# Kernel optimization log

Hardware: AMD Instinct MI355X
Metric: run time of the kernel (lower is better)

## Reference

```python
import jax, jax.numpy as jnp
import numpy as np

B, N = 4, 2466  # batch, vertex count (Pixel2Mesh stage-3 mesh)
IMG = 224.0


def _vertex_align(feat_maps, pos):
    """Bilinear-style gather of image features at projected vertex locations.
    feat_maps: list of [B,C,S,S]; pos: [B,N,3]. Returns [B,N,sum(C)]."""
    z = pos[..., 2]
    h = jnp.clip(248.0 * (pos[..., 1] / z) + 111.5, 0.0, 223.0)
    w = jnp.clip(248.0 * (pos[..., 0] / (-z)) + 111.5, 0.0, 223.0)
    outs = []
    for f in feat_maps:
        S = f.shape[-1]
        x = h / (IMG / S)
        y = w / (IMG / S)
        x1 = jnp.floor(x).astype(jnp.int32)
        x2 = jnp.minimum(jnp.ceil(x).astype(jnp.int32), S - 1)
        y1 = jnp.floor(y).astype(jnp.int32)
        y2 = jnp.minimum(jnp.ceil(y).astype(jnp.int32), S - 1)
        xi = x.astype(jnp.int32)  # trunc == floor since x >= 0
        yi = y.astype(jnp.int32)

        def gat(fm, xs, ys):  # fm [C,S,S], xs/ys [N] -> [N,C]
            return fm[:, xs, ys].T

        g = jax.vmap(gat)
        w11 = ((x2 - xi) * (y2 - yi)).astype(f.dtype)[..., None]
        w12 = ((x2 - xi) * (yi - y1)).astype(f.dtype)[..., None]
        w21 = ((xi - x1) * (y2 - yi)).astype(f.dtype)[..., None]
        w22 = ((xi - x1) * (yi - y1)).astype(f.dtype)[..., None]
        outs.append(w11 * g(f, x1, y1) + w21 * g(f, x2, y1)
                    + w12 * g(f, x1, y2) + w22 * g(f, x2, y2))
    return jnp.concatenate(outs, axis=-1)


def _graph_conv(x, adj, w0, w1):
    # relu(X @ w0 + A @ (X @ w1))
    return jax.nn.relu(x @ w0 + jnp.einsum('bmn,bnc->bmc', adj, x @ w1))


def _res_graph_conv(x, adj, pw, pb, w00, w01, w10, w11):
    skip = x @ pw + pb
    out = _graph_conv(x, adj, w00, w01)
    out = _graph_conv(out, adj, w10, w11)
    return skip + out


def _forward(conv2_3, conv3_4, conv4_6, conv5_3, vertex_positions, vertex_features,
             vertex_adjacency, lin_w, lin_b,
             r0_pw, r0_pb, r0_w00, r0_w01, r0_w10, r0_w11,
             r1_pw, r1_pb, r1_w00, r1_w01, r1_w10, r1_w11,
             r2_pw, r2_pb, r2_w00, r2_w01, r2_w10, r2_w11,
             gf_w0, gf_w1):
    aligned = _vertex_align([conv2_3, conv3_4, conv4_6, conv5_3], vertex_positions)  # [B,N,3840]
    proj = aligned @ lin_w + lin_b  # [B,N,128]
    x = jnp.concatenate([proj, vertex_features, vertex_positions], axis=-1)  # [B,N,259]
    x = _res_graph_conv(x, vertex_adjacency, r0_pw, r0_pb, r0_w00, r0_w01, r0_w10, r0_w11)
    x = _res_graph_conv(x, vertex_adjacency, r1_pw, r1_pb, r1_w00, r1_w01, r1_w10, r1_w11)
    x = _res_graph_conv(x, vertex_adjacency, r2_pw, r2_pb, r2_w00, r2_w01, r2_w10, r2_w11)
    offset = jnp.tanh(_graph_conv(x, vertex_adjacency, gf_w0, gf_w1))  # [B,N,3]
    return vertex_positions + offset


def setup_inputs() -> dict:
    key = jax.random.key(0)
    ks = jax.random.split(key, 40)
    inp = {
        "conv2_3": jax.random.normal(ks[0], (B, 256, 56, 56), jnp.float32),
        "conv3_4": jax.random.normal(ks[1], (B, 512, 28, 28), jnp.float32),
        "conv4_6": jax.random.normal(ks[2], (B, 1024, 14, 14), jnp.float32),
        "conv5_3": jax.random.normal(ks[3], (B, 2048, 7, 7), jnp.float32),
        "vertex_positions": jax.random.normal(ks[4], (B, N, 3), jnp.float32),
        "vertex_features": jax.random.normal(ks[5], (B, N, 128), jnp.float32),
        # sparse 0/1 adjacency stored dense (the torch module uses dense bmm)
        "vertex_adjacency": (jax.random.uniform(ks[6], (B, N, N)) < 0.003).astype(jnp.float32),
    }

    def u(k, shape, fan):
        b = 1.0 / np.sqrt(fan)
        return jax.random.uniform(k, shape, jnp.float32, -b, b)

    specs = [("lin_w", (3840, 128), 3840), ("lin_b", (128,), 3840)]
    for j, ci in enumerate([259, 128, 128]):
        p = f"r{j}_"
        specs += [(p + "pw", (ci, 128), ci), (p + "pb", (128,), ci),
                  (p + "w00", (ci, 128), ci), (p + "w01", (ci, 128), ci),
                  (p + "w10", (128, 128), 128), (p + "w11", (128, 128), 128)]
    specs += [("gf_w0", (128, 3), 128), ("gf_w1", (128, 3), 128)]
    for i, (name, shape, fan) in enumerate(specs):
        inp[name] = u(ks[7 + i], shape, fan)
    return inp


def reference(conv2_3, conv3_4, conv4_6, conv5_3, vertex_positions, vertex_features,
              vertex_adjacency, lin_w, lin_b,
              r0_pw, r0_pb, r0_w00, r0_w01, r0_w10, r0_w11,
              r1_pw, r1_pb, r1_w00, r1_w01, r1_w10, r1_w11,
              r2_pw, r2_pb, r2_w00, r2_w01, r2_w10, r2_w11,
              gf_w0, gf_w1):
    return _forward(conv2_3, conv3_4, conv4_6, conv5_3, vertex_positions, vertex_features,
                    vertex_adjacency, lin_w, lin_b,
                    r0_pw, r0_pb, r0_w00, r0_w01, r0_w10, r0_w11,
                    r1_pw, r1_pb, r1_w00, r1_w01, r1_w10, r1_w11,
                    r2_pw, r2_pb, r2_w00, r2_w01, r2_w10, r2_w11,
                    gf_w0, gf_w1)
```

## Files before the change

kernel.cpp:

```cpp
#include <hip/hip_runtime.h>
#include <cmath>

#define B_   4
#define N_   2466
#define R_   (B_*N_)
#define ELLW 96

typedef _Float16 f16x8 __attribute__((ext_vector_type(8)));
typedef __attribute__((ext_vector_type(4))) float f32x4;

__device__ __forceinline__ unsigned short f16_bits(float x) {
  union { _Float16 h; unsigned short u; } c;
  c.h = (_Float16)x;
  return c.u;
}

struct WMats { const float* p[15]; };


__global__ __launch_bounds__(256) void k_pre(
    const float* __restrict__ c2, const float* __restrict__ c3,
    const float* __restrict__ c4, const float* __restrict__ c5,
    unsigned short* __restrict__ t0, unsigned short* __restrict__ t1,
    unsigned short* __restrict__ t2, unsigned short* __restrict__ t3,
    const float* __restrict__ adj, int* __restrict__ cols, int* __restrict__ cnts,
    const float* __restrict__ lin_w,
    unsigned short* __restrict__ whf,
    WMats wm,
    unsigned short* __restrict__ wrf) {
  __shared__ float t[64][66];
  int bid = blockIdx.x;
  int tid = threadIdx.x;
  if (bid < 1584) {
    const float* in; unsigned short* out; int C, P, npb, ncb, rem;
    if (bid < 784)       { in = c2; out = t0; C = 256;  P = 3136; npb = 49; ncb = 4;  rem = bid; }
    else if (bid < 1200) { in = c3; out = t1; C = 512;  P = 784;  npb = 13; ncb = 8;  rem = bid - 784; }
    else if (bid < 1456) { in = c4; out = t2; C = 1024; P = 196;  npb = 4;  ncb = 16; rem = bid - 1200; }
    else                 { in = c5; out = t3; C = 2048; P = 49;   npb = 1;  ncb = 32; rem = bid - 1456; }
    int pb = rem % npb; int tq = rem / npb; int cb = tq % ncb; int b = tq / ncb;
    int c0 = cb * 64, p0 = pb * 64;
    #pragma unroll
    for (int i = 0; i < 8; i++) {
      int e = tid + i * 256;
      int c = e >> 5, f2 = e & 31;
      int p = p0 + f2 * 2;
      float2 v = make_float2(0.f, 0.f);
      const float* src = in + ((size_t)b * C + (c0 + c)) * P + p;
      if (p + 1 < P)      v = *(const float2*)src;
      else if (p < P)     v.x = *src;
      *(float2*)&t[c][f2 * 2] = v;
    }
    __syncthreads();
    int jj = tid & 15, c4i = jj * 4;
    #pragma unroll
    for (int pass = 0; pass < 4; pass++) {
      int pp = pass * 16 + (tid >> 4);
      int px = p0 + pp;
      if (px < P) {
        ushort4 o;
        o.x = f16_bits(t[c4i + 0][pp]);
        o.y = f16_bits(t[c4i + 1][pp]);
        o.z = f16_bits(t[c4i + 2][pp]);
        o.w = f16_bits(t[c4i + 3][pp]);
        *(ushort4*)&out[((size_t)b * P + px) * C + c0 + c4i] = o;
      }
    }
  } else if (bid < 4050) {
    int wave = tid >> 6, lane = tid & 63;
    int row = (bid - 1584) * 4 + wave;
    const float* Ar = adj + (size_t)row * N_;
    int* cp = cols + (size_t)row * ELLW;
    unsigned long long below = (lane == 63) ? 0xFFFFFFFFFFFFFFFFull >> 1
                                            : ((1ull << lane) - 1ull);
    float4 v[10];
    #pragma unroll
    for (int i0 = 0; i0 < 10; i0++) {
      int j0 = i0 * 256 + lane * 4;
      if (j0 + 3 < N_) {
        v[i0] = *(const float4*)&Ar[j0];
      } else {
        v[i0] = make_float4(0.f, 0.f, 0.f, 0.f);
        if (j0     < N_) v[i0].x = Ar[j0];
        if (j0 + 1 < N_) v[i0].y = Ar[j0+1];
        if (j0 + 2 < N_) v[i0].z = Ar[j0+2];
      }
    }
    int base = 0;
    #pragma unroll
    for (int i0 = 0; i0 < 10; i0++) {
      int j0 = i0 * 256 + lane * 4;
      bool nz0 = (j0     < N_) && (v[i0].x != 0.f);
      bool nz1 = (j0 + 1 < N_) && (v[i0].y != 0.f);
      bool nz2 = (j0 + 2 < N_) && (v[i0].z != 0.f);
      bool nz3 = (j0 + 3 < N_) && (v[i0].w != 0.f);
      unsigned long long m0 = __ballot(nz0);
      unsigned long long m1 = __ballot(nz1);
      unsigned long long m2 = __ballot(nz2);
      unsigned long long m3 = __ballot(nz3);
      int pre = __popcll(m0 & below) + __popcll(m1 & below)
              + __popcll(m2 & below) + __popcll(m3 & below);
      int p0 = base + pre;
      int p1 = p0 + (nz0 ? 1 : 0);
      int p2 = p1 + (nz1 ? 1 : 0);
      int p3 = p2 + (nz2 ? 1 : 0);
      if (nz0 && p0 < ELLW) cp[p0] = j0;
      if (nz1 && p1 < ELLW) cp[p1] = j0 + 1;
      if (nz2 && p2 < ELLW) cp[p2] = j0 + 2;
      if (nz3 && p3 < ELLW) cp[p3] = j0 + 3;
      base += __popcll(m0) + __popcll(m1) + __popcll(m2) + __popcll(m3);
    }
    if (lane == 0) cnts[row] = (base > ELLW) ? ELLW : base;
  } else if (bid < 4530) {
    int b = bid - 4050;
    int e0 = (b * 256 + tid) * 4;
    #pragma unroll
    for (int u = 0; u < 4; u++) {
      int e = e0 + u;
      int j = e & 7;
      int lane = (e >> 3) & 63;
      int nt = (e >> 9) & 7;
      int slab = e >> 12;
      int k = slab * 32 + ((lane >> 4) << 3) + j;
      int n = nt * 16 + (lane & 15);
      whf[e] = f16_bits(lin_w[(size_t)k * 128 + n]);
    }
  } else {
    int b = bid - 4530;
    int e0 = (b * 256 + tid) * 4;
    #pragma unroll
    for (int u = 0; u < 4; u++) {
      int e = e0 + u;
      int rb, mat, rem, K;
      if (e < 143360) {
        rb = 0;
        if (e < 110592) { mat = e / 36864; rem = e - mat * 36864; K = 259; }
        else { int tt = e - 110592; mat = 3 + tt / 16384; rem = tt & 16383; K = 128; }
      } else {
        int tt = e - 143360;
        rb = 1 + tt / 81920;
        int r2 = tt % 81920;
        mat = r2 / 16384; rem = r2 & 16383; K = 128;
      }
      int j = rem & 7, lane = (rem >> 3) & 63, nt = (rem >> 9) & 7, slab = rem >> 12;
      int k = slab * 32 + ((lane >> 4) << 3) + j;
      int n = nt * 16 + (lane & 15);
      float x = (k < K) ? wm.p[rb * 5 + mat][(size_t)k * 128 + n] : 0.f;
      wrf[e] = f16_bits(x);
    }
  }
}

__global__ __launch_bounds__(512) void k_align_mfma(
    const unsigned short* __restrict__ tr0, const unsigned short* __restrict__ tr1,
    const unsigned short* __restrict__ tr2, const unsigned short* __restrict__ tr3,
    const float* __restrict__ pos,
    const unsigned short* __restrict__ whf,
    float* __restrict__ part, int kchunk) {
  int tid  = threadIdx.x;
  int wave = tid >> 6, lane = tid & 63;
  int q    = lane >> 4, l15 = lane & 15;
  int m0   = blockIdx.x * 128;
  int s    = blockIdx.y;
  int mrow = m0 + wave * 16 + l15;

  int zero[4]; int base[4];
  {
    int rowc = (mrow < R_) ? mrow : 0;
    int b = rowc / N_;
    float px = pos[rowc*3+0], py = pos[rowc*3+1], pz = pos[rowc*3+2];
    float hh = fminf(fmaxf(248.f*(py/pz)    + 111.5f, 0.f), 223.f);
    float wc = fminf(fmaxf(248.f*(px/(-pz)) + 111.5f, 0.f), 223.f);
    const int Sarr[4] = {56, 28, 14, 7};
    const int Carr[4] = {256, 512, 1024, 2048};
    #pragma unroll
    for (int sc = 0; sc < 4; sc++) {
      int S = Sarr[sc], C = Carr[sc];
      float dv = 224.f / (float)S;
      float x = hh / dv, y = wc / dv;
      int x1 = (int)floorf(x), y1 = (int)floorf(y);
      int x2 = min((int)ceilf(x), S - 1), y2 = min((int)ceilf(y), S - 1);
      int w = (x2 - x1) * (y2 - y1);
      zero[sc] = (mrow >= R_) || (w == 0);
      base[sc] = (b * S * S + x1 * S + y1) * C;
    }
  }

  f32x4 acc[8];
  #pragma unroll
  for (int nt = 0; nt < 8; nt++) acc[nt] = (f32x4){0.f, 0.f, 0.f, 0.f};

  const f16x8* BH = (const f16x8*)whf;

  int kbeg = s * kchunk, kend = kbeg + kchunk;
  #pragma unroll 1
  for (int k0 = kbeg; k0 < kend; k0 += 32) {
    const unsigned short* tr; int off, sI;
    if (k0 < 256)       { tr = tr0; off = 0;    sI = 0; }
    else if (k0 < 768)  { tr = tr1; off = 256;  sI = 1; }
    else if (k0 < 1792) { tr = tr2; off = 768;  sI = 2; }
    else                { tr = tr3; off = 1792; sI = 3; }

    f16x8 af = *(const f16x8*)(tr + base[sI] + (k0 - off) + q * 8);
    if (zero[sI]) af = (f16x8)(_Float16)0;

    int slab = k0 >> 5;
    f16x8 Bh[8];
    #pragma unroll
    for (int nt = 0; nt < 8; nt++)
      Bh[nt] = BH[(size_t)(slab * 8 + nt) * 64 + lane];
    #pragma unroll
    for (int nt = 0; nt < 8; nt++)
      acc[nt] = __builtin_amdgcn_mfma_f32_16x16x32_f16(af, Bh[nt], acc[nt], 0, 0, 0);
  }

  #pragma unroll
  for (int nt = 0; nt < 8; nt++)
    #pragma unroll
    for (int r = 0; r < 4; r++) {
      int row = m0 + wave * 16 + q * 4 + r;
      if (row < R_)
        part[((size_t)s * R_ + row) * 128 + nt * 16 + l15] = acc[nt][r];
    }
}

__global__ __launch_bounds__(256) void k_reduce(
    const float* __restrict__ part, const float* __restrict__ lin_b,
    const float* __restrict__ vf, const float* __restrict__ pos,
    float* __restrict__ xcat, int nsplit) {
  int grp = threadIdx.x >> 5, ln = threadIdx.x & 31;
  int row = blockIdx.x * 8 + grp;
  float4 acc = ((const float4*)lin_b)[ln];
  for (int s = 0; s < nsplit; s++) {
    float4 pv = ((const float4*)part)[((size_t)s * R_ + row) * 32 + ln];
    acc.x += pv.x; acc.y += pv.y; acc.z += pv.z; acc.w += pv.w;
  }
  float4* xr = (float4*)(xcat + (size_t)row * 288);
  xr[ln] = acc;
  xr[32 + ln] = ((const float4*)vf)[(size_t)row * 32 + ln];
  if (ln < 8) {
    float4 z = make_float4(0.f, 0.f, 0.f, 0.f);
    if (ln == 0) {
      z.x = pos[(size_t)row * 3 + 0];
      z.y = pos[(size_t)row * 3 + 1];
      z.z = pos[(size_t)row * 3 + 2];
    }
    xr[64 + ln] = z;
  }
}

template<int SLABS>
__global__ __launch_bounds__(256) void k_gemm_mfma(
    const float* __restrict__ X, int ldx,
    const unsigned short* __restrict__ wf,
    int matStride, const float* __restrict__ pb,
    float* __restrict__ o0, float* __restrict__ o1, float* __restrict__ o2) {
  int tid = threadIdx.x;
  int wave = tid >> 6, lane = tid & 63;
  int q = lane >> 4, l15 = lane & 15;
  int which = blockIdx.y;
  int m0 = blockIdx.x * 64;
  int mrow = m0 + wave * 16 + l15;
  int rowc = (mrow < R_) ? mrow : (R_ - 1);
  const float* xrow = X + (size_t)rowc * ldx + q * 8;

  const f16x8* BH = (const f16x8*)(wf + (size_t)which * matStride);

  f32x4 acc[8];
  #pragma unroll
  for (int nt = 0; nt < 8; nt++) acc[nt] = (f32x4){0.f, 0.f, 0.f, 0.f};

  #pragma unroll 1
  for (int slab = 0; slab < SLABS; slab++) {
    const float* src = xrow + slab * 32;
    float4 a0 = *(const float4*)src;
    float4 a1 = *(const float4*)(src + 4);
    f16x8 af;
    af[0] = (_Float16)a0.x; af[1] = (_Float16)a0.y;
    af[2] = (_Float16)a0.z; af[3] = (_Float16)a0.w;
    af[4] = (_Float16)a1.x; af[5] = (_Float16)a1.y;
    af[6] = (_Float16)a1.z; af[7] = (_Float16)a1.w;
    f16x8 Bh[8];
    #pragma unroll
    for (int nt = 0; nt < 8; nt++)
      Bh[nt] = BH[(size_t)(slab * 8 + nt) * 64 + lane];
    #pragma unroll
    for (int nt = 0; nt < 8; nt++)
      acc[nt] = __builtin_amdgcn_mfma_f32_16x16x32_f16(af, Bh[nt], acc[nt], 0, 0, 0);
  }

  float* out = (which == 0) ? o0 : (which == 1) ? o1 : o2;
  #pragma unroll
  for (int nt = 0; nt < 8; nt++) {
    int col = nt * 16 + l15;
    float bias = (pb != nullptr && which == 2) ? pb[col] : 0.f;
    #pragma unroll
    for (int r = 0; r < 4; r++) {
      int row = m0 + wave * 16 + q * 4 + r;
      if (row < R_) out[(size_t)row * 128 + col] = acc[nt][r] + bias;
    }
  }
}

__global__ __launch_bounds__(256) void k_spmm(
    const float* __restrict__ sb, const float* __restrict__ tb,
    const int* __restrict__ cols, const int* __restrict__ cnts,
    const float* __restrict__ skipb, float* __restrict__ outb,
    const float* __restrict__ gw0, const float* __restrict__ gw1,
    float* __restrict__ gsb, float* __restrict__ gtb, int fuse_gf) {
  int tid = threadIdx.x;
  int grp = tid >> 5, ln = tid & 31;
  int row = blockIdx.x * 8 + grp;
  int b = row / N_;
  size_t tbase = (size_t)b * N_;
  const float4* sb4 = (const float4*)sb;
  const float4* tb4 = (const float4*)tb;
  const int* cp = cols + (size_t)row * ELLW;
  int4 ci0 = *(const int4*)cp;
  int4 ci1 = *(const int4*)(cp + 4);
  int cnt = cnts[row];
  float4 acc = sb4[(size_t)row*32 + ln];
  int idx[8] = {ci0.x, ci0.y, ci0.z, ci0.w, ci1.x, ci1.y, ci1.z, ci1.w};
  float4 g[8];
  #pragma unroll
  for (int i = 0; i < 8; i++) {
    int c = idx[i];
    c = (c >= 0 && c < N_) ? c : 0;
    g[i] = tb4[(tbase + c)*32 + ln];
  }
  #pragma unroll
  for (int i = 0; i < 8; i++) {
    if (i < cnt) {
      acc.x += g[i].x; acc.y += g[i].y; acc.z += g[i].z; acc.w += g[i].w;
    }
  }
  for (int i = 8; i < cnt; i++) {
    float4 v = tb4[(tbase + cp[i])*32 + ln];
    acc.x += v.x; acc.y += v.y; acc.z += v.z; acc.w += v.w;
  }
  acc.x = fmaxf(acc.x, 0.f); acc.y = fmaxf(acc.y, 0.f);
  acc.z = fmaxf(acc.z, 0.f); acc.w = fmaxf(acc.w, 0.f);
  if (skipb) {
    float4 sv = ((const float4*)skipb)[(size_t)row*32 + ln];
    acc.x += sv.x; acc.y += sv.y; acc.z += sv.z; acc.w += sv.w;
  }
  if (!fuse_gf) {
    ((float4*)outb)[(size_t)row*32 + ln] = acc;
    return;
  }
  float av[4] = {acc.x, acc.y, acc.z, acc.w};
  int j0 = ln * 4;
  float p0 = 0.f, p1 = 0.f, p2 = 0.f, q0 = 0.f, q1 = 0.f, q2 = 0.f;
  #pragma unroll
  for (int u = 0; u < 4; u++) {
    int j = j0 + u;
    p0 += av[u] * gw0[j*3+0]; p1 += av[u] * gw0[j*3+1]; p2 += av[u] * gw0[j*3+2];
    q0 += av[u] * gw1[j*3+0]; q1 += av[u] * gw1[j*3+1]; q2 += av[u] * gw1[j*3+2];
  }
  #pragma unroll
  for (int off = 16; off >= 1; off >>= 1) {
    p0 += __shfl_xor(p0, off); p1 += __shfl_xor(p1, off); p2 += __shfl_xor(p2, off);
    q0 += __shfl_xor(q0, off); q1 += __shfl_xor(q1, off); q2 += __shfl_xor(q2, off);
  }
  if (ln == 0) {
    gsb[(size_t)row*128 + 0] = p0; gsb[(size_t)row*128 + 1] = p1; gsb[(size_t)row*128 + 2] = p2;
    gtb[(size_t)row*128 + 0] = q0; gtb[(size_t)row*128 + 1] = q1; gtb[(size_t)row*128 + 2] = q2;
  }
}

__global__ __launch_bounds__(256) void k_gf_final(
    const float* __restrict__ sb, const float* __restrict__ tb,
    const int* __restrict__ cols, const int* __restrict__ cnts,
    const float* __restrict__ pos, float* __restrict__ out) {
  int wave = threadIdx.x >> 6, lane = threadIdx.x & 63;
  int row = blockIdx.x * 4 + wave;
  if (lane >= 3) return;
  int b = row / N_;
  float acc = sb[(size_t)row*128 + lane];
  int cnt = cnts[row];
  const int* cp = cols + (size_t)row * ELLW;
  size_t tbase = (size_t)b * N_;
  for (int i = 0; i < cnt; i++)
    acc += tb[(tbase + cp[i])*128 + lane];
  float v = tanhf(fmaxf(acc, 0.f));
  out[(size_t)row*3 + lane] = pos[(size_t)row*3 + lane] + v;
}

extern "C" void kernel_launch(void* const* d_in, const int* in_sizes, int n_in,
                              void* d_out, int out_size, void* d_ws, size_t ws_size,
                              hipStream_t stream) {
  const float* conv2_3 = (const float*)d_in[0];
  const float* conv3_4 = (const float*)d_in[1];
  const float* conv4_6 = (const float*)d_in[2];
  const float* conv5_3 = (const float*)d_in[3];
  const float* pos     = (const float*)d_in[4];
  const float* vf      = (const float*)d_in[5];
  const float* adj     = (const float*)d_in[6];
  const float* lin_w   = (const float*)d_in[7];
  const float* lin_b   = (const float*)d_in[8];
  const float* r_pb[3]  = {(const float*)d_in[10], (const float*)d_in[16], (const float*)d_in[22]};
  const float* gf_w0 = (const float*)d_in[27];
  const float* gf_w1 = (const float*)d_in[28];
  float* out = (float*)d_out;

  const size_t TRH_TOT = 6021120;
  const size_t ROWF    = (size_t)R_ * 128;
  const size_t XCAT_F  = (size_t)R_ * 288;
  const size_t LINW_E  = 491520;
  const size_t RESW_E  = 307200;

  unsigned short* trh0 = (unsigned short*)d_ws;
  unsigned short* trh1 = trh0 + (size_t)4*256*3136;
  unsigned short* trh2 = trh1 + (size_t)4*512*784;
  unsigned short* trh3 = trh2 + (size_t)4*1024*196;
  int*   ell_cnt  = (int*)(trh3 + (size_t)4*2048*49);
  int*   ell_cols = ell_cnt + R_;
  unsigned short* whf = (unsigned short*)(ell_cols + (size_t)R_*ELLW);
  unsigned short* wrf = whf + LINW_E;
  float* part = (float*)(wrf + RESW_E + 512);

  size_t fixed_f = TRH_TOT/2 + (size_t)R_*(ELLW+1) + (LINW_E + RESW_E + 512)/2;
  size_t need8 = (fixed_f + (size_t)8*ROWF + XCAT_F + 5*ROWF) * sizeof(float);
  int nsplit = (ws_size >= need8) ? 8 : 4;
  int kchunk = 3840 / nsplit;

  float* xcat = part + (size_t)nsplit * ROWF;
  float* sb   = xcat + XCAT_F;
  float* tb   = sb   + ROWF;
  float* skip = tb   + ROWF;
  float* hb   = skip + ROWF;
  float* xc   = hb   + ROWF;

  WMats wm;
  for (int rb = 0; rb < 3; rb++) {
    wm.p[rb*5 + 0] = (const float*)d_in[11 + 6*rb];
    wm.p[rb*5 + 1] = (const float*)d_in[12 + 6*rb];
    wm.p[rb*5 + 2] = (const float*)d_in[9  + 6*rb];
    wm.p[rb*5 + 3] = (const float*)d_in[13 + 6*rb];
    wm.p[rb*5 + 4] = (const float*)d_in[14 + 6*rb];
  }
  const int RB_BASE[3] = {0, 143360, 225280};

  k_pre<<<4830, 256, 0, stream>>>(conv2_3, conv3_4, conv4_6, conv5_3,
                                  trh0, trh1, trh2, trh3,
                                  adj, ell_cols, ell_cnt,
                                  lin_w, whf, wm, wrf);

  k_align_mfma<<<dim3(78, nsplit), 512, 0, stream>>>(trh0, trh1, trh2, trh3, pos,
                                                     whf, part, kchunk);

  k_reduce<<<1233, 256, 0, stream>>>(part, lin_b, vf, pos, xcat, nsplit);

  for (int rb = 0; rb < 3; rb++) {
    if (rb == 0) {
      k_gemm_mfma<9><<<dim3(155, 3), 256, 0, stream>>>(
          xcat, 288, wrf + RB_BASE[0], 36864, r_pb[0], sb, tb, skip);
    } else {
      k_gemm_mfma<4><<<dim3(155, 3), 256, 0, stream>>>(
          xc, 128, wrf + RB_BASE[rb], 16384, r_pb[rb], sb, tb, skip);
    }
    k_spmm<<<1233, 256, 0, stream>>>(sb, tb, ell_cols, ell_cnt, nullptr, hb,
                                     nullptr, nullptr, nullptr, nullptr, 0);
    int g2off = RB_BASE[rb] + ((rb == 0) ? 110592 : 3 * 16384);
    k_gemm_mfma<4><<<dim3(155, 2), 256, 0, stream>>>(
        hb, 128, wrf + g2off, 16384, nullptr, sb, tb, nullptr);
    if (rb < 2) {
      k_spmm<<<1233, 256, 0, stream>>>(sb, tb, ell_cols, ell_cnt, skip, xc,
                                       nullptr, nullptr, nullptr, nullptr, 0);
    } else {
      k_spmm<<<1233, 256, 0, stream>>>(sb, tb, ell_cols, ell_cnt, skip, nullptr,
                                       gf_w0, gf_w1, hb, xc, 1);
    }
  }

  k_gf_final<<<2466, 256, 0, stream>>>(hb, xc, ell_cols, ell_cnt, pos, out);
}
```

Before: 428.1 us.

## Process two row tiles per wave in align GEMM and prefetch more ELL neighbors

The vertex-align MFMA kernel now runs 4 waves per block, each covering two 16-row tiles, so every B-fragment load from the weight matrix feeds two MFMAs. This halves redundant weight traffic per row and raises the number of independent MFMAs in flight per wave, at the cost of more accumulator registers. The SpMM and final graph-conv kernels also issue 12 neighbor gathers up front instead of 8 (or a serial loop), to expose more memory-level parallelism for typical vertex degrees.

```diff
diff --git a/kernel.cpp b/kernel.cpp
--- a/kernel.cpp
+++ b/kernel.cpp
@@ -150,7 +150,7 @@
   }
 }
 
-__global__ __launch_bounds__(512) void k_align_mfma(
+__global__ __launch_bounds__(256) void k_align_mfma(
     const unsigned short* __restrict__ tr0, const unsigned short* __restrict__ tr1,
     const unsigned short* __restrict__ tr2, const unsigned short* __restrict__ tr3,
     const float* __restrict__ pos,
@@ -161,10 +161,11 @@
   int q    = lane >> 4, l15 = lane & 15;
   int m0   = blockIdx.x * 128;
   int s    = blockIdx.y;
-  int mrow = m0 + wave * 16 + l15;
-
-  int zero[4]; int base[4];
-  {
+
+  int zero[2][4]; int base[2][4];
+  #pragma unroll
+  for (int u = 0; u < 2; u++) {
+    int mrow = m0 + (wave * 2 + u) * 16 + l15;
     int rowc = (mrow < R_) ? mrow : 0;
     int b = rowc / N_;
     float px = pos[rowc*3+0], py = pos[rowc*3+1], pz = pos[rowc*3+2];
@@ -180,14 +181,16 @@
       int x1 = (int)floorf(x), y1 = (int)floorf(y);
       int x2 = min((int)ceilf(x), S - 1), y2 = min((int)ceilf(y), S - 1);
       int w = (x2 - x1) * (y2 - y1);
-      zero[sc] = (mrow >= R_) || (w == 0);
-      base[sc] = (b * S * S + x1 * S + y1) * C;
-    }
-  }
-
-  f32x4 acc[8];
-  #pragma unroll
-  for (int nt = 0; nt < 8; nt++) acc[nt] = (f32x4){0.f, 0.f, 0.f, 0.f};
+      zero[u][sc] = (mrow >= R_) || (w == 0);
+      base[u][sc] = (b * S * S + x1 * S + y1) * C;
+    }
+  }
+
+  f32x4 acc[2][8];
+  #pragma unroll
+  for (int u = 0; u < 2; u++)
+    #pragma unroll
+    for (int nt = 0; nt < 8; nt++) acc[u][nt] = (f32x4){0.f, 0.f, 0.f, 0.f};
 
   const f16x8* BH = (const f16x8*)whf;
 
@@ -200,8 +203,12 @@
     else if (k0 < 1792) { tr = tr2; off = 768;  sI = 2; }
     else                { tr = tr3; off = 1792; sI = 3; }
 
-    f16x8 af = *(const f16x8*)(tr + base[sI] + (k0 - off) + q * 8);
-    if (zero[sI]) af = (f16x8)(_Float16)0;
+    f16x8 af[2];
+    #pragma unroll
+    for (int u = 0; u < 2; u++) {
+      af[u] = *(const f16x8*)(tr + base[u][sI] + (k0 - off) + q * 8);
+      if (zero[u][sI]) af[u] = (f16x8)(_Float16)0;
+    }
 
     int slab = k0 >> 5;
     f16x8 Bh[8];
@@ -209,18 +216,22 @@
     for (int nt = 0; nt < 8; nt++)
       Bh[nt] = BH[(size_t)(slab * 8 + nt) * 64 + lane];
     #pragma unroll
+    for (int nt = 0; nt < 8; nt++) {
+      acc[0][nt] = __builtin_amdgcn_mfma_f32_16x16x32_f16(af[0], Bh[nt], acc[0][nt], 0, 0, 0);
+      acc[1][nt] = __builtin_amdgcn_mfma_f32_16x16x32_f16(af[1], Bh[nt], acc[1][nt], 0, 0, 0);
+    }
+  }
+
+  #pragma unroll
+  for (int u = 0; u < 2; u++)
+    #pragma unroll
     for (int nt = 0; nt < 8; nt++)
-      acc[nt] = __builtin_amdgcn_mfma_f32_16x16x32_f16(af, Bh[nt], acc[nt], 0, 0, 0);
-  }
-
-  #pragma unroll
-  for (int nt = 0; nt < 8; nt++)
-    #pragma unroll
-    for (int r = 0; r < 4; r++) {
-      int row = m0 + wave * 16 + q * 4 + r;
-      if (row < R_)
-        part[((size_t)s * R_ + row) * 128 + nt * 16 + l15] = acc[nt][r];
-    }
+      #pragma unroll
+      for (int r = 0; r < 4; r++) {
+        int row = m0 + (wave * 2 + u) * 16 + q * 4 + r;
+        if (row < R_)
+          part[((size_t)s * R_ + row) * 128 + nt * 16 + l15] = acc[u][nt][r];
+      }
 }
 
 __global__ __launch_bounds__(256) void k_reduce(
@@ -317,23 +328,25 @@
   const int* cp = cols + (size_t)row * ELLW;
   int4 ci0 = *(const int4*)cp;
   int4 ci1 = *(const int4*)(cp + 4);
+  int4 ci2 = *(const int4*)(cp + 8);
   int cnt = cnts[row];
   float4 acc = sb4[(size_t)row*32 + ln];
-  int idx[8] = {ci0.x, ci0.y, ci0.z, ci0.w, ci1.x, ci1.y, ci1.z, ci1.w};
-  float4 g[8];
-  #pragma unroll
-  for (int i = 0; i < 8; i++) {
+  int idx[12] = {ci0.x, ci0.y, ci0.z, ci0.w, ci1.x, ci1.y, ci1.z, ci1.w,
+                 ci2.x, ci2.y, ci2.z, ci2.w};
+  float4 g[12];
+  #pragma unroll
+  for (int i = 0; i < 12; i++) {
     int c = idx[i];
     c = (c >= 0 && c < N_) ? c : 0;
     g[i] = tb4[(tbase + c)*32 + ln];
   }
   #pragma unroll
-  for (int i = 0; i < 8; i++) {
+  for (int i = 0; i < 12; i++) {
     if (i < cnt) {
       acc.x += g[i].x; acc.y += g[i].y; acc.z += g[i].z; acc.w += g[i].w;
     }
   }
-  for (int i = 8; i < cnt; i++) {
+  for (int i = 12; i < cnt; i++) {
     float4 v = tb4[(tbase + cp[i])*32 + ln];
     acc.x += v.x; acc.y += v.y; acc.z += v.z; acc.w += v.w;
   }
@@ -375,11 +388,26 @@
   int row = blockIdx.x * 4 + wave;
   if (lane >= 3) return;
   int b = row / N_;
+  size_t tbase = (size_t)b * N_;
+  const int* cp = cols + (size_t)row * ELLW;
+  int4 ci0 = *(const int4*)cp;
+  int4 ci1 = *(const int4*)(cp + 4);
+  int4 ci2 = *(const int4*)(cp + 8);
+  int cnt = cnts[row];
   float acc = sb[(size_t)row*128 + lane];
-  int cnt = cnts[row];
-  const int* cp = cols + (size_t)row * ELLW;
-  size_t tbase = (size_t)b * N_;
-  for (int i = 0; i < cnt; i++)
+  int idx[12] = {ci0.x, ci0.y, ci0.z, ci0.w, ci1.x, ci1.y, ci1.z, ci1.w,
+                 ci2.x, ci2.y, ci2.z, ci2.w};
+  float g[12];
+  #pragma unroll
+  for (int i = 0; i < 12; i++) {
+    int c = idx[i];
+    c = (c >= 0 && c < N_) ? c : 0;
+    g[i] = tb[(tbase + c)*128 + lane];
+  }
+  #pragma unroll
+  for (int i = 0; i < 12; i++)
+    if (i < cnt) acc += g[i];
+  for (int i = 12; i < cnt; i++)
     acc += tb[(tbase + cp[i])*128 + lane];
   float v = tanhf(fmaxf(acc, 0.f));
   out[(size_t)row*3 + lane] = pos[(size_t)row*3 + lane] + v;
@@ -445,7 +473,7 @@
                                   adj, ell_cols, ell_cnt,
                                   lin_w, whf, wm, wrf);
 
-  k_align_mfma<<<dim3(78, nsplit), 512, 0, stream>>>(trh0, trh1, trh2, trh3, pos,
+  k_align_mfma<<<dim3(78, nsplit), 256, 0, stream>>>(trh0, trh1, trh2, trh3, pos,
                                                      whf, part, kchunk);
 
   k_reduce<<<1233, 256, 0, stream>>>(part, lin_b, vf, pos, xcat, nsplit);
```

Measured after the change: 411.6 us. -3.8%, faster.
